# Kernel optimization log

Measured on AMD Instinct MI355X. Metric: run time of the kernel, lower is better.

The kernel has to match this reference:

```python
import jax, jax.numpy as jnp
import numpy as np

B, S, E, H = 4, 1024, 1024, 16
HD = E // H  # 64


def setup_inputs() -> dict:
    key = jax.random.key(0)
    ks = jax.random.split(key, 9)
    scale = 1.0 / np.sqrt(E)
    x = jax.random.normal(ks[0], (B, S, E), dtype=jnp.float32)
    attention_mask = jnp.ones((B, S, S), dtype=jnp.int32)
    # per-head projection weights, batched over heads: [H, E, HD]
    Wq = jax.random.normal(ks[1], (H, E, HD), dtype=jnp.float32) * scale
    Wk = jax.random.normal(ks[2], (H, E, HD), dtype=jnp.float32) * scale
    Wv = jax.random.normal(ks[3], (H, E, HD), dtype=jnp.float32) * scale
    bq = jax.random.normal(ks[4], (H, HD), dtype=jnp.float32) * scale
    bk = jax.random.normal(ks[5], (H, HD), dtype=jnp.float32) * scale
    bv = jax.random.normal(ks[6], (H, HD), dtype=jnp.float32) * scale
    # output projection, torch Linear convention: [out_features, in_features]
    Wo = jax.random.normal(ks[7], (E, E), dtype=jnp.float32) * scale
    bo = jax.random.normal(ks[8], (E,), dtype=jnp.float32) * scale
    return {"x": x, "attention_mask": attention_mask, "Wq": Wq, "bq": bq,
            "Wk": Wk, "bk": bk, "Wv": Wv, "bv": bv, "Wo": Wo, "bo": bo}


def reference(x, attention_mask, Wq, bq, Wk, bk, Wv, bv, Wo, bo):
    # batched-over-heads QKV projections: (B,S,E) x (H,E,HD) -> (B,H,S,HD)
    q = jnp.einsum('bse,hed->bhsd', x, Wq) + bq[None, :, None, :]
    k = jnp.einsum('bse,hed->bhsd', x, Wk) + bk[None, :, None, :]
    v = jnp.einsum('bse,hed->bhsd', x, Wv) + bv[None, :, None, :]
    scores = jnp.einsum('bhsd,bhtd->bhst', q, k) / jnp.sqrt(jnp.float32(HD))
    mask = attention_mask[:, None, :, :]  # (B,1,S,S) broadcast over heads
    scores = jnp.where(mask == 0, -jnp.inf, scores)
    weights = jax.nn.softmax(scores, axis=-1)
    out = jnp.einsum('bhst,bhtd->bhsd', weights, v)
    # concat heads on last dim: (B,S,H*HD) == (B,S,E)
    out = out.transpose(0, 2, 1, 3).reshape(B, S, E)
    return out @ Wo.T + bo
```

## Files before the change

kernel.cpp:

```cpp
#include <hip/hip_runtime.h>
#include <hip/hip_bf16.h>

#define NB 4
#define SEQ 1024
#define EMB 1024
#define NH 16
#define HD 64

typedef unsigned short u16;
typedef __attribute__((ext_vector_type(8))) __bf16 bf16x8;
typedef __attribute__((ext_vector_type(8))) short short8;
typedef __attribute__((ext_vector_type(4))) float floatx4;

__device__ inline u16 f2b_rn(float f) {
    union { float f; unsigned int i; } x; x.f = f;
    unsigned int r = (x.i + 0x7FFFu + ((x.i >> 16) & 1u)) >> 16;
    return (u16)r;
}
__device__ inline bf16x8 s2b(short8 v) {
    union { short8 s; bf16x8 b; } x; x.s = v; return x.b;
}

__device__ inline void gload_lds16(const void* g, void* l) {
    __builtin_amdgcn_global_load_lds(
        (const __attribute__((address_space(1))) void*)g,
        (__attribute__((address_space(3))) void*)l, 16, 0, 0);
}

__device__ inline bf16x8 ldsfrag(const u16* base, int r, int c) {
    return s2b(*(const short8*)&base[r * 64 + (c ^ ((r & 7) * 8))]);
}

__device__ inline void cvt8(const float* __restrict__ s, u16* __restrict__ d) {
    float4 a = *(const float4*)(s);
    float4 b = *(const float4*)(s + 4);
    union { u16 u[8]; int4 v; } o;
    o.u[0] = f2b_rn(a.x); o.u[1] = f2b_rn(a.y); o.u[2] = f2b_rn(a.z); o.u[3] = f2b_rn(a.w);
    o.u[4] = f2b_rn(b.x); o.u[5] = f2b_rn(b.y); o.u[6] = f2b_rn(b.z); o.u[7] = f2b_rn(b.w);
    *(int4*)(d) = o.v;
}

__global__ __launch_bounds__(256) void prep(
    const float* __restrict__ x, const float* __restrict__ Wq,
    const float* __restrict__ Wk, const float* __restrict__ Wv,
    const int* __restrict__ mask,
    u16* __restrict__ xb, u16* __restrict__ Wt,
    unsigned long long* __restrict__ bits)
{
    __shared__ u16 T[64 * 80];
    int bx = blockIdx.x;
    int tid = threadIdx.x;

    if (bx < 512) {
        #pragma unroll
        for (int c = 0; c < 4; ++c) {
            int i = (bx * 4 + c) * 2048 + tid * 8;
            cvt8(x + i, xb + i);
        }
    } else if (bx < 1280) {
        int bx2 = bx - 512;
        int e0 = (bx2 & 15) * 64;
        int ph = bx2 >> 4;
        int p = ph >> 4, h = ph & 15;
        const float* W = (p == 0 ? Wq : (p == 1 ? Wk : Wv)) + h * (EMB * HD);
        #pragma unroll
        for (int c = 0; c < 2; ++c) {
            int flat = c * 2048 + tid * 8;
            int r = flat >> 6;
            int d = flat & 63;
            cvt8(W + (size_t)(e0 + r) * HD + d, &T[r * 80 + d]);
        }
        __syncthreads();
        int d = tid >> 2;
        int ec = tid & 3;
        union { u16 u[16]; int4 v[2]; } tmp;
        #pragma unroll
        for (int i = 0; i < 16; ++i) tmp.u[i] = T[(ec * 16 + i) * 80 + d];
        u16* dst = Wt + ((size_t)(p * NH + h) * HD + d) * EMB + e0 + ec * 16;
        *(int4*)(dst) = tmp.v[0];
        *(int4*)(dst + 8) = tmp.v[1];
    } else {
        int base = (bx - 1280) * 16 + (tid >> 6) * 4;
        int lane = tid & 63;
        #pragma unroll
        for (int i = 0; i < 4; ++i) {
            int gw = base + i;
            int m = mask[(size_t)gw * 64 + lane];
            unsigned long long bl = __ballot(m != 0);
            if (lane == 0) bits[gw] = bl;
        }
    }
}

__global__ __launch_bounds__(256) void qkv_gemm(
    const u16* __restrict__ x,
    const u16* __restrict__ Wt2,
    const float* __restrict__ bq, const float* __restrict__ bk, const float* __restrict__ bv,
    u16* __restrict__ Q, u16* __restrict__ K, u16* __restrict__ Vt)
{
    __shared__ u16 As[128 * 64];
    __shared__ u16 Bs[128 * 64];

    int gid = blockIdx.x;
    int xcd = gid & 7;
    int j   = gid >> 3;
    int mt_ = (xcd & 3) * 8 + (j & 7);
    int nt_ = (xcd >> 2) * 12 + (j >> 3);
    int m0 = mt_ * 128;
    int n0 = nt_ * 128;

    int tid = threadIdx.x;
    int w = tid >> 6, lane = tid & 63, quad = lane >> 4, ln = lane & 15;
    int wm = w & 1, wn = w >> 1;

    floatx4 acc[4][4] = {};

    for (int k0 = 0; k0 < EMB; k0 += 64) {
        __syncthreads();
        #pragma unroll
        for (int i = 0; i < 4; ++i) {
            int flat0 = i * 256 + (tid & 192);
            int flat = flat0 + lane;
            int r = flat >> 3;
            int c = ((flat & 7) ^ (r & 7)) * 8;
            gload_lds16(x   + (size_t)(m0 + r) * EMB + k0 + c, As + flat0 * 8);
            gload_lds16(Wt2 + (size_t)(n0 + r) * EMB + k0 + c, Bs + flat0 * 8);
        }
        __syncthreads();

        #pragma unroll
        for (int kk = 0; kk < 2; ++kk) {
            bf16x8 a[4], bf[4];
            #pragma unroll
            for (int mt = 0; mt < 4; ++mt)
                a[mt] = ldsfrag(As, wm * 64 + mt * 16 + ln, kk * 32 + quad * 8);
            #pragma unroll
            for (int nc = 0; nc < 4; ++nc)
                bf[nc] = ldsfrag(Bs, wn * 64 + nc * 16 + ln, kk * 32 + quad * 8);
            #pragma unroll
            for (int mt = 0; mt < 4; ++mt)
                #pragma unroll
                for (int nc = 0; nc < 4; ++nc)
                    acc[mt][nc] = __builtin_amdgcn_mfma_f32_16x16x32_bf16(a[mt], bf[nc], acc[mt][nc], 0, 0, 0);
        }
    }

    int p = n0 >> 10;
    const float* bias = (p == 0 ? bq : (p == 1 ? bk : bv));
    if (p < 2) {
        u16* Out = (p == 0) ? Q : K;
        float qs = (p == 0) ? 0.125f * 1.44269504f : 1.0f;
        #pragma unroll
        for (int nc = 0; nc < 4; ++nc) {
            int n = n0 + wn * 64 + nc * 16 + ln;
            int h = (n >> 6) & 15, d = n & 63;
            float bv_ = bias[n & 1023];
            #pragma unroll
            for (int mt = 0; mt < 4; ++mt) {
                #pragma unroll
                for (int reg = 0; reg < 4; ++reg) {
                    int m = m0 + wm * 64 + mt * 16 + quad * 4 + reg;
                    int b_ = m >> 10, s = m & 1023;
                    Out[((size_t)(b_ * NH + h) * SEQ + s) * HD + d] = f2b_rn((acc[mt][nc][reg] + bv_) * qs);
                }
            }
        }
    } else {
        #pragma unroll
        for (int nc = 0; nc < 4; ++nc) {
            int n = n0 + wn * 64 + nc * 16 + ln;
            int h = (n >> 6) & 15, d = n & 63;
            float bv_ = bias[n & 1023];
            #pragma unroll
            for (int mt = 0; mt < 4; ++mt) {
                int m = m0 + wm * 64 + mt * 16 + quad * 4;
                int b_ = m >> 10, s = m & 1023;
                union { u16 u[4]; uint2 v; } pk;
                #pragma unroll
                for (int reg = 0; reg < 4; ++reg)
                    pk.u[reg] = f2b_rn(acc[mt][nc][reg] + bv_);
                *(uint2*)&Vt[((size_t)(b_ * NH + h) * HD + d) * SEQ + s] = pk.v;
            }
        }
    }
}

__global__ __launch_bounds__(256) void attn(
    const u16* __restrict__ Q, const u16* __restrict__ K, const u16* __restrict__ Vt,
    const unsigned long long* __restrict__ bits,
    const float* __restrict__ Wo, u16* __restrict__ Wob,
    u16* __restrict__ Aout)
{
    const int PP = 72;
    __shared__ u16 Ks[64 * 64];
    __shared__ u16 Vs[80 * 64];
    __shared__ u16 Ps[128 * PP];

    int bid = blockIdx.x;
    int tid = threadIdx.x;

    if (bid >= 512) {
        int i = (bid - 512) * 2048 + tid * 8;
        cvt8(Wo + i, Wob + i);
        return;
    }

    int bh = bid & 63;
    int q0 = (bid >> 6) * 128;
    int b = bh >> 4, h = bh & 15;
    const u16* Qb = Q  + (size_t)bh * SEQ * HD;
    const u16* Kb = K  + (size_t)bh * SEQ * HD;
    const u16* Vb = Vt + (size_t)bh * HD * SEQ;

    int w = tid >> 6, lane = tid & 63, quad = lane >> 4, ln = lane & 15;

    if (tid < 16) *(uint2*)&Vs[64 * 64 + tid * 4] = make_uint2(0x3F803F80u, 0x3F803F80u);

    bf16x8 qf[2][2];
    #pragma unroll
    for (int s = 0; s < 2; ++s) {
        const u16* qp = Qb + (size_t)(q0 + w * 32 + s * 16 + ln) * HD + quad * 8;
        union { int4 i; bf16x8 b; } c0, c1;
        c0.i = *(const int4*)(qp);
        c1.i = *(const int4*)(qp + 32);
        qf[s][0] = c0.b; qf[s][1] = c1.b;
    }

    floatx4 o[2][5] = {};

    for (int tt = 0; tt < SEQ / 64; ++tt) {
        int t0 = tt * 64;
        __syncthreads();
        #pragma unroll
        for (int i = 0; i < 2; ++i) {
            int flat0 = i * 256 + (tid & 192);
            int flat = flat0 + lane;
            int r = flat >> 3;
            int c = ((flat & 7) ^ (r & 7)) * 8;
            gload_lds16(Kb + (size_t)(t0 + r) * HD + c, Ks + flat0 * 8);
            gload_lds16(Vb + (size_t)r * SEQ + t0 + c, Vs + flat0 * 8);
        }
        __syncthreads();

        floatx4 sc[2][4] = {};
        #pragma unroll
        for (int kk = 0; kk < 2; ++kk) {
            bf16x8 kf[4];
            #pragma unroll
            for (int tb = 0; tb < 4; ++tb)
                kf[tb] = ldsfrag(Ks, tb * 16 + ln, kk * 32 + quad * 8);
            #pragma unroll
            for (int s = 0; s < 2; ++s)
                #pragma unroll
                for (int tb = 0; tb < 4; ++tb)
                    sc[s][tb] = __builtin_amdgcn_mfma_f32_16x16x32_bf16(kf[tb], qf[s][kk], sc[s][tb], 0, 0, 0);
        }

        #pragma unroll
        for (int s = 0; s < 2; ++s) {
            unsigned long long bm = bits[((size_t)b * SEQ + q0 + w * 32 + s * 16 + ln) * 16 + tt];
            if (__any(bm != ~0ull)) {
                #pragma unroll
                for (int tb = 0; tb < 4; ++tb)
                    #pragma unroll
                    for (int reg = 0; reg < 4; ++reg)
                        if (!((bm >> (tb * 16 + quad * 4 + reg)) & 1)) sc[s][tb][reg] = -1e30f;
            }
        }

        #pragma unroll
        for (int s = 0; s < 2; ++s) {
            int mrow = w * 32 + s * 16 + ln;
            #pragma unroll
            for (int tb = 0; tb < 4; ++tb) {
                union { float f; unsigned int i; } e0_, e1_, e2_, e3_;
                e0_.f = __builtin_amdgcn_exp2f(sc[s][tb][0]);
                e1_.f = __builtin_amdgcn_exp2f(sc[s][tb][1]);
                e2_.f = __builtin_amdgcn_exp2f(sc[s][tb][2]);
                e3_.f = __builtin_amdgcn_exp2f(sc[s][tb][3]);
                uint2 pk;
                pk.x = ((e0_.i + 0x8000u) >> 16) | ((e1_.i + 0x8000u) & 0xFFFF0000u);
                pk.y = ((e2_.i + 0x8000u) >> 16) | ((e3_.i + 0x8000u) & 0xFFFF0000u);
                *(uint2*)&Ps[mrow * PP + tb * 16 + quad * 4] = pk;
            }
        }

        #pragma unroll
        for (int kk = 0; kk < 2; ++kk) {
            bf16x8 vf[5];
            #pragma unroll
            for (int dt = 0; dt < 5; ++dt)
                vf[dt] = ldsfrag(Vs, dt * 16 + ln, kk * 32 + quad * 8);
            #pragma unroll
            for (int s = 0; s < 2; ++s) {
                bf16x8 pf = s2b(*(const short8*)&Ps[(w * 32 + s * 16 + ln) * PP + kk * 32 + quad * 8]);
                #pragma unroll
                for (int dt = 0; dt < 5; ++dt)
                    o[s][dt] = __builtin_amdgcn_mfma_f32_16x16x32_bf16(pf, vf[dt], o[s][dt], 0, 0, 0);
            }
        }
    }

    #pragma unroll
    for (int s = 0; s < 2; ++s) {
        #pragma unroll
        for (int reg = 0; reg < 4; ++reg) {
            float l = __shfl(o[s][4][reg], lane & 48, 64);
            float inv = 1.0f / l;
            int m = q0 + w * 32 + s * 16 + quad * 4 + reg;
            #pragma unroll
            for (int dt = 0; dt < 4; ++dt)
                Aout[((size_t)b * SEQ + m) * EMB + h * HD + dt * 16 + ln] = f2b_rn(o[s][dt][reg] * inv);
        }
    }
}

__global__ __launch_bounds__(256) void out_proj(
    const u16* __restrict__ A,
    const u16* __restrict__ Wo,
    const float* __restrict__ bo,
    float* __restrict__ Out)
{
    __shared__ u16 As[64 * 64];
    __shared__ u16 Bs[128 * 64];

    int gid = blockIdx.x;
    int xcd = gid & 7;
    int j   = gid >> 3;
    int m0 = (xcd * 8 + (j & 7)) * 64;
    int n0 = (j >> 3) * 128;

    int tid = threadIdx.x;
    int w = tid >> 6, lane = tid & 63, quad = lane >> 4, ln = lane & 15;
    int wm = w & 1, wn = w >> 1;

    floatx4 acc[2][4] = {};

    for (int k0 = 0; k0 < EMB; k0 += 64) {
        __syncthreads();
        #pragma unroll
        for (int i = 0; i < 2; ++i) {
            int flat0 = i * 256 + (tid & 192);
            int flat = flat0 + lane;
            int r = flat >> 3;
            int c = ((flat & 7) ^ (r & 7)) * 8;
            gload_lds16(A + (size_t)(m0 + r) * EMB + k0 + c, As + flat0 * 8);
        }
        #pragma unroll
        for (int i = 0; i < 4; ++i) {
            int flat0 = i * 256 + (tid & 192);
            int flat = flat0 + lane;
            int r = flat >> 3;
            int c = ((flat & 7) ^ (r & 7)) * 8;
            gload_lds16(Wo + (size_t)(n0 + r) * EMB + k0 + c, Bs + flat0 * 8);
        }
        __syncthreads();

        #pragma unroll
        for (int kk = 0; kk < 2; ++kk) {
            bf16x8 a[2], bfr[4];
            #pragma unroll
            for (int mt = 0; mt < 2; ++mt)
                a[mt] = ldsfrag(As, wm * 32 + mt * 16 + ln, kk * 32 + quad * 8);
            #pragma unroll
            for (int nc = 0; nc < 4; ++nc)
                bfr[nc] = ldsfrag(Bs, wn * 64 + nc * 16 + ln, kk * 32 + quad * 8);
            #pragma unroll
            for (int mt = 0; mt < 2; ++mt)
                #pragma unroll
                for (int nc = 0; nc < 4; ++nc)
                    acc[mt][nc] = __builtin_amdgcn_mfma_f32_16x16x32_bf16(a[mt], bfr[nc], acc[mt][nc], 0, 0, 0);
        }
    }

    #pragma unroll
    for (int nc = 0; nc < 4; ++nc) {
        int n = n0 + wn * 64 + nc * 16 + ln;
        float bb = bo[n];
        #pragma unroll
        for (int mt = 0; mt < 2; ++mt) {
            #pragma unroll
            for (int reg = 0; reg < 4; ++reg) {
                int m = m0 + wm * 32 + mt * 16 + quad * 4 + reg;
                Out[(size_t)m * EMB + n] = acc[mt][nc][reg] + bb;
            }
        }
    }
}

extern "C" void kernel_launch(void* const* d_in, const int* in_sizes, int n_in,
                              void* d_out, int out_size, void* d_ws, size_t ws_size,
                              hipStream_t stream) {
    const float* x  = (const float*)d_in[0];
    const int*   mk = (const int*)d_in[1];
    const float* Wq = (const float*)d_in[2];
    const float* bq = (const float*)d_in[3];
    const float* Wk = (const float*)d_in[4];
    const float* bk = (const float*)d_in[5];
    const float* Wv = (const float*)d_in[6];
    const float* bv = (const float*)d_in[7];
    const float* Wo = (const float*)d_in[8];
    const float* bo = (const float*)d_in[9];
    float* out = (float*)d_out;

    const size_t MB = 1u << 20;
    char* ws = (char*)d_ws;
    u16* xb  = (u16*)ws;
    u16* Wt  = (u16*)(ws + 8 * MB);
    u16* Wob = (u16*)(ws + 14 * MB);
    unsigned long long* bits = (unsigned long long*)(ws + 16 * MB);
    u16* Qw  = (u16*)(ws + 16 * MB + 512 * 1024);
    u16* Kw  = (u16*)(ws + 24 * MB + 512 * 1024);
    u16* Vtw = (u16*)(ws + 32 * MB + 512 * 1024);
    u16* Ao  = xb;

    prep<<<5376, 256, 0, stream>>>(x, Wq, Wk, Wv, mk, xb, Wt, bits);
    qkv_gemm<<<768, 256, 0, stream>>>(xb, Wt, bq, bk, bv, Qw, Kw, Vtw);
    attn<<<1024, 256, 0, stream>>>(Qw, Kw, Vtw, bits, Wo, Wob, Ao);
    out_proj<<<512, 256, 0, stream>>>(Ao, Wob, bo, out);
}
```

Measured before the change: 195.8 us.

## Rewrite QKV GEMM with 256x256 tiles and 8-wave interleaved LDS pipeline

The QKV projection GEMM now uses 256x256 output tiles per 512-thread block, with double-buffered A/B tiles in 128KB of LDS. Global-to-LDS loads for upcoming K-steps are interleaved between MFMA sub-blocks, using explicit vmcnt waits, barriers and setprio. The aim is more operand reuse per load and overlap of memory traffic with matrix math. In exchange the grid drops to 192 blocks, fewer than the CU count, so occupancy and load balance get worse.

```diff
diff --git a/kernel.cpp b/kernel.cpp
--- a/kernel.cpp
+++ b/kernel.cpp
@@ -92,93 +92,163 @@
     }
 }
 
-__global__ __launch_bounds__(256) void qkv_gemm(
+#define BARX do { __builtin_amdgcn_sched_barrier(0); __builtin_amdgcn_s_barrier(); __builtin_amdgcn_sched_barrier(0); } while(0)
+#define VMCNT6 asm volatile("s_waitcnt vmcnt(6)" ::: "memory")
+#define VMCNT0 asm volatile("s_waitcnt vmcnt(0)" ::: "memory")
+
+__device__ __forceinline__ void rd_b(const u16* B, int wn, int ln, int quad, bf16x8 (&bfr)[4][2]) {
+    #pragma unroll
+    for (int nc = 0; nc < 4; ++nc) {
+        bfr[nc][0] = ldsfrag(B, wn * 64 + nc * 16 + ln, quad * 8);
+        bfr[nc][1] = ldsfrag(B, wn * 64 + nc * 16 + ln, 32 + quad * 8);
+    }
+}
+__device__ __forceinline__ void rd_a(const u16* A, int wm, int mf0, int ln, int quad, bf16x8 (&a)[2][2]) {
+    #pragma unroll
+    for (int jj = 0; jj < 2; ++jj) {
+        a[jj][0] = ldsfrag(A, wm * 128 + (mf0 + jj) * 16 + ln, quad * 8);
+        a[jj][1] = ldsfrag(A, wm * 128 + (mf0 + jj) * 16 + ln, 32 + quad * 8);
+    }
+}
+__device__ __forceinline__ void mm8(floatx4 (&acc)[8][4], const bf16x8 (&a)[2][2],
+                                    const bf16x8 (&bfr)[4][2], int mf0) {
+    #pragma unroll
+    for (int jj = 0; jj < 2; ++jj)
+        #pragma unroll
+        for (int nc = 0; nc < 4; ++nc) {
+            acc[mf0 + jj][nc] = __builtin_amdgcn_mfma_f32_16x16x32_bf16(a[jj][0], bfr[nc][0], acc[mf0 + jj][nc], 0, 0, 0);
+            acc[mf0 + jj][nc] = __builtin_amdgcn_mfma_f32_16x16x32_bf16(a[jj][1], bfr[nc][1], acc[mf0 + jj][nc], 0, 0, 0);
+        }
+}
+
+#define STG(srcb, buf, c, kt) gload_lds16((srcb) + (size_t)(c) * 65536 + (kt) * 64 + soff, (buf) + (c) * 4096 + ldst)
+
+__global__ __launch_bounds__(512, 2) void qkv_gemm(
     const u16* __restrict__ x,
     const u16* __restrict__ Wt2,
     const float* __restrict__ bq, const float* __restrict__ bk, const float* __restrict__ bv,
     u16* __restrict__ Q, u16* __restrict__ K, u16* __restrict__ Vt)
 {
-    __shared__ u16 As[128 * 64];
-    __shared__ u16 Bs[128 * 64];
+    __shared__ u16 L[65536];
+    u16* A0s = L;
+    u16* A1s = L + 16384;
+    u16* B0s = L + 32768;
+    u16* B1s = L + 49152;
 
     int gid = blockIdx.x;
     int xcd = gid & 7;
     int j   = gid >> 3;
-    int mt_ = (xcd & 3) * 8 + (j & 7);
-    int nt_ = (xcd >> 2) * 12 + (j >> 3);
-    int m0 = mt_ * 128;
-    int n0 = nt_ * 128;
+    int mt_ = (xcd >> 1) * 4 + (j & 3);
+    int nt_ = (xcd & 1) * 6 + (j >> 2);
+    int m0 = mt_ * 256;
+    int n0 = nt_ * 256;
 
     int tid = threadIdx.x;
     int w = tid >> 6, lane = tid & 63, quad = lane >> 4, ln = lane & 15;
-    int wm = w & 1, wn = w >> 1;
-
-    floatx4 acc[4][4] = {};
-
-    for (int k0 = 0; k0 < EMB; k0 += 64) {
-        __syncthreads();
-        #pragma unroll
-        for (int i = 0; i < 4; ++i) {
-            int flat0 = i * 256 + (tid & 192);
-            int flat = flat0 + lane;
-            int r = flat >> 3;
-            int c = ((flat & 7) ^ (r & 7)) * 8;
-            gload_lds16(x   + (size_t)(m0 + r) * EMB + k0 + c, As + flat0 * 8);
-            gload_lds16(Wt2 + (size_t)(n0 + r) * EMB + k0 + c, Bs + flat0 * 8);
-        }
-        __syncthreads();
-
-        #pragma unroll
-        for (int kk = 0; kk < 2; ++kk) {
-            bf16x8 a[4], bf[4];
-            #pragma unroll
-            for (int mt = 0; mt < 4; ++mt)
-                a[mt] = ldsfrag(As, wm * 64 + mt * 16 + ln, kk * 32 + quad * 8);
-            #pragma unroll
-            for (int nc = 0; nc < 4; ++nc)
-                bf[nc] = ldsfrag(Bs, wn * 64 + nc * 16 + ln, kk * 32 + quad * 8);
-            #pragma unroll
-            for (int mt = 0; mt < 4; ++mt)
-                #pragma unroll
-                for (int nc = 0; nc < 4; ++nc)
-                    acc[mt][nc] = __builtin_amdgcn_mfma_f32_16x16x32_bf16(a[mt], bf[nc], acc[mt][nc], 0, 0, 0);
-        }
-    }
-
-    int p = n0 >> 10;
+    int wm = w >> 2, wn = w & 3;
+
+    const u16* Asrc = x   + (size_t)m0 * EMB;
+    const u16* Bsrc = Wt2 + (size_t)n0 * EMB;
+
+    int sr = tid >> 3;
+    int sc = ((tid & 7) ^ (sr & 7)) * 8;
+    size_t soff = (size_t)sr * EMB + sc;
+    int ldst = w * 512;
+
+    STG(Asrc, A0s, 0, 0); STG(Asrc, A0s, 1, 0); STG(Asrc, A0s, 2, 0); STG(Asrc, A0s, 3, 0);
+    STG(Bsrc, B0s, 0, 0); STG(Bsrc, B0s, 1, 0); STG(Bsrc, B0s, 2, 0); STG(Bsrc, B0s, 3, 0);
+    STG(Bsrc, B1s, 0, 1); STG(Bsrc, B1s, 1, 1); STG(Bsrc, B1s, 2, 1); STG(Bsrc, B1s, 3, 1);
+    STG(Asrc, A1s, 0, 1); STG(Asrc, A1s, 2, 1);
+    VMCNT6;
+    BARX;
+
+    floatx4 acc[8][4] = {};
+    bf16x8 bfr[4][2];
+    bf16x8 a[2][2];
+
+    for (int i = 0; i < 8; ++i) {
+        const int T = 2 * i;
+        const bool st = (i < 7);
+        rd_b(B0s, wn, ln, quad, bfr);
+        rd_a(A0s, wm, 0, ln, quad, a);
+        STG(Asrc, A1s, 1, T + 1); STG(Asrc, A1s, 3, T + 1);
+        BARX;
+        __builtin_amdgcn_s_setprio(1); mm8(acc, a, bfr, 0); __builtin_amdgcn_s_setprio(0);
+        BARX;
+        rd_a(A0s, wm, 2, ln, quad, a);
+        if (st) { STG(Bsrc, B0s, 0, T + 2); STG(Bsrc, B0s, 1, T + 2); }
+        BARX;
+        __builtin_amdgcn_s_setprio(1); mm8(acc, a, bfr, 2); __builtin_amdgcn_s_setprio(0);
+        BARX;
+        rd_a(A0s, wm, 4, ln, quad, a);
+        if (st) { STG(Bsrc, B0s, 2, T + 2); STG(Bsrc, B0s, 3, T + 2); }
+        BARX;
+        __builtin_amdgcn_s_setprio(1); mm8(acc, a, bfr, 4); __builtin_amdgcn_s_setprio(0);
+        BARX;
+        rd_a(A0s, wm, 6, ln, quad, a);
+        if (st) { STG(Asrc, A0s, 0, T + 2); STG(Asrc, A0s, 2, T + 2); }
+        BARX;
+        __builtin_amdgcn_s_setprio(1); mm8(acc, a, bfr, 6); __builtin_amdgcn_s_setprio(0);
+        if (st) { VMCNT6; } else { VMCNT0; }
+        BARX;
+        rd_b(B1s, wn, ln, quad, bfr);
+        rd_a(A1s, wm, 0, ln, quad, a);
+        if (st) { STG(Asrc, A0s, 1, T + 2); STG(Asrc, A0s, 3, T + 2); }
+        BARX;
+        __builtin_amdgcn_s_setprio(1); mm8(acc, a, bfr, 0); __builtin_amdgcn_s_setprio(0);
+        BARX;
+        rd_a(A1s, wm, 2, ln, quad, a);
+        if (st) { STG(Bsrc, B1s, 0, T + 3); STG(Bsrc, B1s, 1, T + 3); }
+        BARX;
+        __builtin_amdgcn_s_setprio(1); mm8(acc, a, bfr, 2); __builtin_amdgcn_s_setprio(0);
+        BARX;
+        rd_a(A1s, wm, 4, ln, quad, a);
+        if (st) { STG(Bsrc, B1s, 2, T + 3); STG(Bsrc, B1s, 3, T + 3); }
+        BARX;
+        __builtin_amdgcn_s_setprio(1); mm8(acc, a, bfr, 4); __builtin_amdgcn_s_setprio(0);
+        BARX;
+        rd_a(A1s, wm, 6, ln, quad, a);
+        if (st) { STG(Asrc, A1s, 0, T + 3); STG(Asrc, A1s, 2, T + 3); }
+        BARX;
+        __builtin_amdgcn_s_setprio(1); mm8(acc, a, bfr, 6); __builtin_amdgcn_s_setprio(0);
+        if (st) { VMCNT6; }
+        BARX;
+    }
+
+    int nbase = n0 + wn * 64;
+    int p = nbase >> 10;
+    int h = (nbase >> 6) & 15;
     const float* bias = (p == 0 ? bq : (p == 1 ? bk : bv));
     if (p < 2) {
         u16* Out = (p == 0) ? Q : K;
         float qs = (p == 0) ? 0.125f * 1.44269504f : 1.0f;
         #pragma unroll
         for (int nc = 0; nc < 4; ++nc) {
-            int n = n0 + wn * 64 + nc * 16 + ln;
-            int h = (n >> 6) & 15, d = n & 63;
-            float bv_ = bias[n & 1023];
-            #pragma unroll
-            for (int mt = 0; mt < 4; ++mt) {
+            int d = nc * 16 + ln;
+            float bv_ = bias[(nbase & 1023) + d];
+            #pragma unroll
+            for (int mf = 0; mf < 8; ++mf) {
                 #pragma unroll
                 for (int reg = 0; reg < 4; ++reg) {
-                    int m = m0 + wm * 64 + mt * 16 + quad * 4 + reg;
+                    int m = m0 + wm * 128 + mf * 16 + quad * 4 + reg;
                     int b_ = m >> 10, s = m & 1023;
-                    Out[((size_t)(b_ * NH + h) * SEQ + s) * HD + d] = f2b_rn((acc[mt][nc][reg] + bv_) * qs);
+                    Out[((size_t)(b_ * NH + h) * SEQ + s) * HD + d] = f2b_rn((acc[mf][nc][reg] + bv_) * qs);
                 }
             }
         }
     } else {
         #pragma unroll
         for (int nc = 0; nc < 4; ++nc) {
-            int n = n0 + wn * 64 + nc * 16 + ln;
-            int h = (n >> 6) & 15, d = n & 63;
-            float bv_ = bias[n & 1023];
-            #pragma unroll
-            for (int mt = 0; mt < 4; ++mt) {
-                int m = m0 + wm * 64 + mt * 16 + quad * 4;
+            int d = nc * 16 + ln;
+            float bv_ = bias[(nbase & 1023) + d];
+            #pragma unroll
+            for (int mf = 0; mf < 8; ++mf) {
+                int m = m0 + wm * 128 + mf * 16 + quad * 4;
                 int b_ = m >> 10, s = m & 1023;
                 union { u16 u[4]; uint2 v; } pk;
                 #pragma unroll
                 for (int reg = 0; reg < 4; ++reg)
-                    pk.u[reg] = f2b_rn(acc[mt][nc][reg] + bv_);
+                    pk.u[reg] = f2b_rn(acc[mf][nc][reg] + bv_);
                 *(uint2*)&Vt[((size_t)(b_ * NH + h) * HD + d) * SEQ + s] = pk.v;
             }
         }
@@ -415,7 +485,7 @@
     u16* Ao  = xb;
 
     prep<<<5376, 256, 0, stream>>>(x, Wq, Wk, Wv, mk, xb, Wt, bits);
-    qkv_gemm<<<768, 256, 0, stream>>>(xb, Wt, bq, bk, bv, Qw, Kw, Vtw);
+    qkv_gemm<<<192, 512, 0, stream>>>(xb, Wt, bq, bk, bv, Qw, Kw, Vtw);
     attn<<<1024, 256, 0, stream>>>(Qw, Kw, Vtw, bits, Wo, Wob, Ao);
     out_proj<<<512, 256, 0, stream>>>(Ao, Wob, bo, out);
 }
```

Result: faster. 185.5 us (-5.3%).
